# Kernel tuning notes

Measured on AMD Instinct MI355X. Metric: run time of the kernel, lower is better.

Reference implementation:

```python
import jax, jax.numpy as jnp
import numpy as np

D_IN = 1024
D_OUT = 1024
NUM_HEADS = 16
HEAD_DIM = D_OUT // NUM_HEADS


def setup_inputs() -> dict:
    key = jax.random.key(0)
    ks = jax.random.split(key, 6)
    B, T = 2, 2048
    x = jax.random.normal(ks[0], (B, T, D_IN), dtype=jnp.float32)
    s = 1.0 / np.sqrt(D_IN)
    Wq = jax.random.normal(ks[1], (D_IN, D_OUT), dtype=jnp.float32) * s
    Wk = jax.random.normal(ks[2], (D_IN, D_OUT), dtype=jnp.float32) * s
    Wv = jax.random.normal(ks[3], (D_IN, D_OUT), dtype=jnp.float32) * s
    Wo = jax.random.normal(ks[4], (D_OUT, D_OUT), dtype=jnp.float32) * (1.0 / np.sqrt(D_OUT))
    bo = jnp.zeros((D_OUT,), dtype=jnp.float32)
    return {"x": x, "Wq": Wq, "Wk": Wk, "Wv": Wv, "Wo": Wo, "bo": bo}


def reference(x, Wq, Wk, Wv, Wo, bo):
    B, T, _ = x.shape
    # project and split heads -> (B, H, T, Dh)
    def split(t):
        return t.reshape(B, T, NUM_HEADS, HEAD_DIM).transpose(0, 2, 1, 3)
    Q = split(x @ Wq)
    K = split(x @ Wk)
    V = split(x @ Wv)
    scale = HEAD_DIM ** -0.5
    scores = jnp.einsum('bhqd,bhkd->bhqk', Q, K) * scale  # (B,H,T,T)
    causal = jnp.triu(jnp.ones((T, T), dtype=bool), k=1)
    scores = jnp.where(causal, -jnp.inf, scores)
    weights = jax.nn.softmax(scores, axis=-1)
    ctx = jnp.einsum('bhqk,bhkd->bhqd', weights, V)  # (B,H,T,Dh)
    ctx = ctx.transpose(0, 2, 1, 3).reshape(B, T, D_OUT)
    return ctx @ Wo + bo
```

## Files before the change

### kernel.cpp

```cpp
#include <hip/hip_runtime.h>
#include <hip/hip_bf16.h>

#define NH   16
#define HD   64
#define BB   2
#define TT   2048
#define DIN  1024
#define DOUT 1024
#define MTOT (BB*TT)

#define QSCALE 0.18033688011112042f
#define MAXC   20.0f

typedef __hip_bfloat16 bf16;
typedef short bf16x8  __attribute__((ext_vector_type(8)));
typedef float f32x4   __attribute__((ext_vector_type(4)));
typedef float f32x16  __attribute__((ext_vector_type(16)));

__device__ __forceinline__ bf16 f2bf(float f){ return __float2bfloat16(f); }

__device__ __forceinline__ void gld16(const bf16* g, bf16* l){
    __builtin_amdgcn_global_load_lds(
        (const __attribute__((address_space(1))) unsigned int*)g,
        (__attribute__((address_space(3))) unsigned int*)l,
        16, 0, 0);
}

__device__ __forceinline__ size_t qk_off(int bh, int t, int d){
    return (size_t)bh*131072 + (size_t)(((t>>5)*4 + (d>>4))*512)
         + ((t&31) + 32*((d>>3)&1))*8 + (d&7);
}
__device__ __forceinline__ size_t v_off(int bh, int t, int d){
    return (size_t)bh*131072 + (size_t)((((t>>4)*2) + (d>>5))*512)
         + ((d&31) + 32*((t>>2)&1))*8 + ((t&3) + 4*((t>>3)&1));
}

__global__ void prep_all(const float* __restrict__ x,
                         const float* __restrict__ Wq, const float* __restrict__ Wk,
                         const float* __restrict__ Wv, const float* __restrict__ Wo,
                         bf16* __restrict__ xb, bf16* __restrict__ WT){
    __shared__ float tile[64][65];
    const int blk = blockIdx.x;
    if (blk < 4096){
        int i = blk*256 + threadIdx.x;
        float4 v = ((const float4*)x)[i];
        bf16 o[4] = {f2bf(v.x), f2bf(v.y), f2bf(v.z), f2bf(v.w)};
        *(ushort4*)&xb[(size_t)i*4] = *(ushort4*)o;
        return;
    }
    const int wb = blk - 4096;
    const int n0 = (wb >> 4) * 64, k0 = (wb & 15) * 64;
    const float* W;
    switch (n0 >> 10){ case 0: W=Wq; break; case 1: W=Wk; break; case 2: W=Wv; break; default: W=Wo; }
    const int c0 = n0 & 1023;
    const int tr = threadIdx.x >> 6;
    const int tc = threadIdx.x & 63;
    #pragma unroll
    for (int it = 0; it < 16; it++){
        int k = k0 + it*4 + tr;
        tile[it*4 + tr][tc] = W[(size_t)k*DOUT + c0 + tc];
    }
    __syncthreads();
    #pragma unroll
    for (int it = 0; it < 16; it++){
        int n = it*4 + tr;
        WT[(size_t)(n0 + n)*DIN + k0 + tc] = f2bf(tile[tc][n]);
    }
}

__launch_bounds__(512, 2)
__global__ void gemm_qkv(const bf16* __restrict__ Xb, const bf16* __restrict__ WT,
                         bf16* __restrict__ Qf, bf16* __restrict__ Kf, bf16* __restrict__ Vf){
    __shared__ __align__(16) bf16 As[2*256*64];
    __shared__ __align__(16) bf16 Bs[2*192*64];
    const int n0 = blockIdx.x * 192;
    const int m0 = blockIdx.y * 256;
    const int tid = threadIdx.x;
    const int wave = tid >> 6, lane = tid & 63;
    const int wr = wave >> 1;
    const int wc = wave & 1;
    const int quad = lane >> 4, l16 = lane & 15;
    const int srow = tid >> 3;
    const int schk = tid & 7;
    const int gcol = (schk ^ (srow & 7)) << 3;

    f32x4 acc[4][6] = {};

    auto stage = [&](int kt, int dbuf){
        const int k0 = kt * 64;
        bf16* Ad = &As[dbuf * 16384];
        bf16* Bd = &Bs[dbuf * 12288];
        #pragma unroll
        for (int j = 0; j < 4; j++){
            int r = srow + j*64;
            gld16(&Xb[(size_t)(m0 + r)*DIN + k0 + gcol], Ad + r*64 + schk*8);
        }
        #pragma unroll
        for (int j = 0; j < 3; j++){
            int r = srow + j*64;
            gld16(&WT[(size_t)(n0 + r)*DIN + k0 + gcol], Bd + r*64 + schk*8);
        }
    };

    auto compute = [&](int dbuf){
        const bf16* Ab = &As[dbuf * 16384];
        const bf16* Bb = &Bs[dbuf * 12288];
        bf16x8 af[4][2];
        #pragma unroll
        for (int mi = 0; mi < 4; mi++){
            int row = wr*64 + mi*16 + l16;
            af[mi][0] = *(const bf16x8*)&Ab[row*64 + (((quad    ) ^ (row & 7)) << 3)];
            af[mi][1] = *(const bf16x8*)&Ab[row*64 + (((4 + quad) ^ (row & 7)) << 3)];
        }
        #pragma unroll
        for (int ni = 0; ni < 6; ni++){
            int row = wc*96 + ni*16 + l16;
            bf16x8 b0 = *(const bf16x8*)&Bb[row*64 + (((quad    ) ^ (row & 7)) << 3)];
            bf16x8 b1 = *(const bf16x8*)&Bb[row*64 + (((4 + quad) ^ (row & 7)) << 3)];
            #pragma unroll
            for (int mi = 0; mi < 4; mi++){
                acc[mi][ni] = __builtin_amdgcn_mfma_f32_16x16x32_bf16(af[mi][0], b0, acc[mi][ni], 0, 0, 0);
                acc[mi][ni] = __builtin_amdgcn_mfma_f32_16x16x32_bf16(af[mi][1], b1, acc[mi][ni], 0, 0, 0);
            }
        }
    };

    stage(0, 0);

    for (int t = 0; t < 15; t++){
        const int buf = t & 1;
        stage(t + 1, buf ^ 1);
        asm volatile("s_waitcnt vmcnt(7)" ::: "memory");
        __builtin_amdgcn_s_barrier();
        compute(buf);
        asm volatile("s_waitcnt lgkmcnt(0)" ::: "memory");
        __builtin_amdgcn_s_barrier();
    }
    asm volatile("s_waitcnt vmcnt(0)" ::: "memory");
    __builtin_amdgcn_s_barrier();
    compute(1);

    #pragma unroll
    for (int mi = 0; mi < 4; mi++){
        #pragma unroll
        for (int ni = 0; ni < 6; ni++){
            int col = n0 + wc*96 + ni*16 + l16;
            int which = col >> 10;
            int c = col & 1023;
            int h = c >> 6, d = c & 63;
            int m_base = m0 + wr*64 + mi*16 + quad*4;
            int b = m_base >> 11, t0 = m_base & 2047;
            int bh = b*NH + h;
            if (which == 2){
                bf16 pk[4];
                #pragma unroll
                for (int r = 0; r < 4; r++) pk[r] = f2bf(acc[mi][ni][r]);
                *(ushort4*)&Vf[v_off(bh, t0, d)] = *(ushort4*)pk;
            } else if (which == 0){
                #pragma unroll
                for (int r = 0; r < 4; r++)
                    Qf[qk_off(bh, t0 + r, d)] = f2bf(acc[mi][ni][r] * QSCALE);
            } else {
                #pragma unroll
                for (int r = 0; r < 4; r++)
                    Kf[qk_off(bh, t0 + r, d)] = f2bf(acc[mi][ni][r]);
            }
        }
    }
}

__launch_bounds__(256, 4)
__global__ void attn(const bf16* __restrict__ Qf, const bf16* __restrict__ Kf,
                     const bf16* __restrict__ Vf, bf16* __restrict__ ctx){
    __shared__ float Lo[3*64*36];
    __shared__ float Ls[3*64];
    const int blk  = blockIdx.x;
    const int bh   = (blk & 7) + 8*((blk >> 3) & 3);
    const int qb   = 63 - (blk >> 5);
    const int wave = threadIdx.x >> 6, lane = threadIdx.x & 63;
    const int n    = qb + 1;
    const int tstart = (n*wave) >> 2;
    const int tend   = ((n*(wave+1)) >> 2) - 1;
    const int h32  = lane >> 5, l32 = lane & 31;
    const int b    = bh >> 4, head = bh & 15;
    const bf16* Qb = Qf + (size_t)bh*131072 + lane*8;
    const bf16* Kb = Kf + (size_t)bh*131072 + lane*8;
    const bf16* Vb = Vf + (size_t)bh*131072 + lane*8;

    bf16x8 qf[4];
    #pragma unroll
    for (int ks = 0; ks < 4; ks++)
        qf[ks] = *(const bf16x8*)(Qb + (qb*4 + ks)*512);

    bf16x8 kc[4], vc[4];
    #pragma unroll
    for (int i = 0; i < 4; i++){
        kc[i] = *(const bf16x8*)(Kb + (tstart*4 + i)*512);
        vc[i] = *(const bf16x8*)(Vb + (tstart*4 + i)*512);
    }

    f32x16 o0 = {}, o1 = {};
    float lsum = 0.f;

    for (int tb = tstart; tb <= tend; tb++){
        f32x16 s = {};
        #pragma unroll
        for (int ks = 0; ks < 4; ks++)
            s = __builtin_amdgcn_mfma_f32_32x32x16_bf16(kc[ks], qf[ks], s, 0, 0, 0);
        if (tb < tend){
            #pragma unroll
            for (int i = 0; i < 4; i++)
                kc[i] = *(const bf16x8*)(Kb + ((tb+1)*4 + i)*512);
        }
        if (tb == qb){
            #pragma unroll
            for (int r = 0; r < 16; r++){
                int trow = (r&3) + 8*(r>>2) + 4*h32;
                if (trow > l32) s[r] = -1e30f;
            }
        }
        float p[16];
        #pragma unroll
        for (int r = 0; r < 16; r++){
            p[r] = __builtin_amdgcn_exp2f(s[r] - MAXC);
            lsum += p[r];
        }
        #pragma unroll
        for (int ki = 0; ki < 2; ki++){
            bf16 pb[8];
            #pragma unroll
            for (int j = 0; j < 8; j++) pb[j] = f2bf(p[ki*8 + j]);
            bf16x8 pbv = *(bf16x8*)pb;
            o0 = __builtin_amdgcn_mfma_f32_32x32x16_bf16(vc[ki*2+0], pbv, o0, 0, 0, 0);
            o1 = __builtin_amdgcn_mfma_f32_32x32x16_bf16(vc[ki*2+1], pbv, o1, 0, 0, 0);
        }
        if (tb < tend){
            #pragma unroll
            for (int i = 0; i < 4; i++)
                vc[i] = *(const bf16x8*)(Vb + ((tb+1)*4 + i)*512);
        }
    }

    if (wave != 0){
        float* lo = &Lo[(wave-1)*2304 + lane*36];
        #pragma unroll
        for (int c = 0; c < 4; c++){
            f32x4 w4 = { o0[c*4+0], o0[c*4+1], o0[c*4+2], o0[c*4+3] };
            *(f32x4*)&lo[c*4] = w4;
        }
        #pragma unroll
        for (int c = 0; c < 4; c++){
            f32x4 w4 = { o1[c*4+0], o1[c*4+1], o1[c*4+2], o1[c*4+3] };
            *(f32x4*)&lo[16 + c*4] = w4;
        }
        Ls[(wave-1)*64 + lane] = lsum;
    }
    __syncthreads();
    if (wave == 0){
        float lc = lsum;
        #pragma unroll
        for (int w = 0; w < 3; w++){
            const float* lo = &Lo[w*2304 + lane*36];
            #pragma unroll
            for (int c = 0; c < 4; c++){
                f32x4 r4 = *(const f32x4*)&lo[c*4];
                #pragma unroll
                for (int i = 0; i < 4; i++) o0[c*4+i] += r4[i];
            }
            #pragma unroll
            for (int c = 0; c < 4; c++){
                f32x4 r4 = *(const f32x4*)&lo[16 + c*4];
                #pragma unroll
                for (int i = 0; i < 4; i++) o1[c*4+i] += r4[i];
            }
            lc += Ls[w*64 + lane];
        }
        float lq  = lc + __shfl_xor(lc, 32);
        float inv = 1.0f / lq;
        const int q = qb*32 + l32;
        bf16* cp = ctx + ((size_t)(b*TT + q))*DOUT + head*HD;
        #pragma unroll
        for (int db = 0; db < 2; db++){
            #pragma unroll
            for (int rq = 0; rq < 4; rq++){
                bf16 pk[4];
                #pragma unroll
                for (int i = 0; i < 4; i++){
                    float ov = (db ? o1[rq*4 + i] : o0[rq*4 + i]) * inv;
                    pk[i] = f2bf(ov);
                }
                int d0 = db*32 + rq*8 + h32*4;
                *(ushort4*)&cp[d0] = *(ushort4*)pk;
            }
        }
    }
}

__launch_bounds__(256)
__global__ void gemm_out(const bf16* __restrict__ Cx, const bf16* __restrict__ WoT,
                         const float* __restrict__ bo, float* __restrict__ out){
    __shared__ __align__(16) bf16 As[128*64];
    __shared__ __align__(16) bf16 Bs[64*64];
    const int n0 = blockIdx.x * 64;
    const int m0 = blockIdx.y * 128;
    const int tid = threadIdx.x;
    const int wave = tid >> 6, lane = tid & 63;
    const int wm = (wave & 1) * 64, wn = (wave >> 1) * 32;
    const int quad = lane >> 4, l16 = lane & 15;
    const int srow = wave*8 + (lane >> 3);
    const int schk = lane & 7;

    f32x4 acc[4][2] = {};
    for (int k0 = 0; k0 < DOUT; k0 += 64){
        #pragma unroll
        for (int j = 0; j < 4; j++){
            int r = srow + j*32;
            int gc = (schk ^ (r & 7)) << 3;
            gld16(&Cx[(size_t)(m0 + r)*DOUT + k0 + gc], &As[r*64 + schk*8]);
        }
        #pragma unroll
        for (int j = 0; j < 2; j++){
            int r = srow + j*32;
            int gc = (schk ^ (r & 7)) << 3;
            gld16(&WoT[(size_t)(n0 + r)*DOUT + k0 + gc], &Bs[r*64 + schk*8]);
        }
        __syncthreads();
        #pragma unroll
        for (int ks = 0; ks < 2; ks++){
            bf16x8 af[4], bfr[2];
            #pragma unroll
            for (int mi = 0; mi < 4; mi++){
                int row = wm + mi*16 + l16;
                af[mi] = *(bf16x8*)&As[row*64 + (((ks*4 + quad) ^ (row & 7)) << 3)];
            }
            #pragma unroll
            for (int ni = 0; ni < 2; ni++){
                int row = wn + ni*16 + l16;
                bfr[ni] = *(bf16x8*)&Bs[row*64 + (((ks*4 + quad) ^ (row & 7)) << 3)];
            }
            #pragma unroll
            for (int mi = 0; mi < 4; mi++)
                #pragma unroll
                for (int ni = 0; ni < 2; ni++)
                    acc[mi][ni] = __builtin_amdgcn_mfma_f32_16x16x32_bf16(af[mi], bfr[ni], acc[mi][ni], 0, 0, 0);
        }
        __syncthreads();
    }
    #pragma unroll
    for (int mi = 0; mi < 4; mi++){
        #pragma unroll
        for (int ni = 0; ni < 2; ni++){
            int nn = n0 + wn + ni*16 + l16;
            float bias = bo[nn];
            #pragma unroll
            for (int r = 0; r < 4; r++){
                int m = m0 + wm + mi*16 + quad*4 + r;
                out[(size_t)m*DOUT + nn] = acc[mi][ni][r] + bias;
            }
        }
    }
}

extern "C" void kernel_launch(void* const* d_in, const int* in_sizes, int n_in,
                              void* d_out, int out_size, void* d_ws, size_t ws_size,
                              hipStream_t stream){
    const float* x  = (const float*)d_in[0];
    const float* Wq = (const float*)d_in[1];
    const float* Wk = (const float*)d_in[2];
    const float* Wv = (const float*)d_in[3];
    const float* Wo = (const float*)d_in[4];
    const float* bo = (const float*)d_in[5];
    float* out = (float*)d_out;

    char* ws = (char*)d_ws;
    bf16* xb  = (bf16*)(ws);
    bf16* WT  = (bf16*)(ws + ((size_t)8  << 20));
    bf16* Qf  = (bf16*)(ws + ((size_t)16 << 20));
    bf16* Kf  = (bf16*)(ws + ((size_t)24 << 20));
    bf16* Vf  = (bf16*)(ws + ((size_t)32 << 20));
    bf16* ctx = (bf16*)(ws + ((size_t)40 << 20));
    bf16* WoT = WT + (size_t)3072*DIN;

    prep_all <<<dim3(5120),    256, 0, stream>>>(x, Wq, Wk, Wv, Wo, xb, WT);
    gemm_qkv <<<dim3(16, 16),  512, 0, stream>>>(xb, WT, Qf, Kf, Vf);
    attn     <<<dim3(2048),    256, 0, stream>>>(Qf, Kf, Vf, ctx);
    gemm_out <<<dim3(16, 32),  256, 0, stream>>>(ctx, WoT, bo, out);
}
```

Before: 164.5 us.

## Double-buffer output projection GEMM and widen tile to 128x128

The output projection GEMM now uses two LDS buffers so the next K tile's global-to-LDS loads are issued before computing on the current tile, with explicit vmcnt waits and barriers. The N tile grows from 64 to 128, so each wave accumulates a 4x4 block of MFMA outputs and the grid halves to 8x32 blocks. This aims to hide load latency and raise operand reuse per LDS read. The cost is more LDS and accumulator registers per block (launch bounds ask for 2 blocks/CU) and fewer blocks in flight.

```diff
diff --git a/kernel.cpp b/kernel.cpp
--- a/kernel.cpp
+++ b/kernel.cpp
@@ -296,60 +296,77 @@
     }
 }
 
-__launch_bounds__(256)
+__launch_bounds__(256, 2)
 __global__ void gemm_out(const bf16* __restrict__ Cx, const bf16* __restrict__ WoT,
                          const float* __restrict__ bo, float* __restrict__ out){
-    __shared__ __align__(16) bf16 As[128*64];
-    __shared__ __align__(16) bf16 Bs[64*64];
-    const int n0 = blockIdx.x * 64;
+    __shared__ __align__(16) bf16 As[2*128*64];
+    __shared__ __align__(16) bf16 Bs[2*128*64];
+    const int n0 = blockIdx.x * 128;
     const int m0 = blockIdx.y * 128;
     const int tid = threadIdx.x;
     const int wave = tid >> 6, lane = tid & 63;
-    const int wm = (wave & 1) * 64, wn = (wave >> 1) * 32;
+    const int wm = (wave & 1) * 64, wn = (wave >> 1) * 64;
     const int quad = lane >> 4, l16 = lane & 15;
-    const int srow = wave*8 + (lane >> 3);
-    const int schk = lane & 7;
-
-    f32x4 acc[4][2] = {};
-    for (int k0 = 0; k0 < DOUT; k0 += 64){
+    const int srow = tid >> 3;
+    const int schk = tid & 7;
+    const int gcol = (schk ^ (srow & 7)) << 3;
+
+    f32x4 acc[4][4] = {};
+
+    auto stage = [&](int kt, int dbuf){
+        const int k0 = kt * 64;
+        bf16* Ad = &As[dbuf * 8192];
+        bf16* Bd = &Bs[dbuf * 8192];
         #pragma unroll
         for (int j = 0; j < 4; j++){
             int r = srow + j*32;
-            int gc = (schk ^ (r & 7)) << 3;
-            gld16(&Cx[(size_t)(m0 + r)*DOUT + k0 + gc], &As[r*64 + schk*8]);
-        }
-        #pragma unroll
-        for (int j = 0; j < 2; j++){
-            int r = srow + j*32;
-            int gc = (schk ^ (r & 7)) << 3;
-            gld16(&WoT[(size_t)(n0 + r)*DOUT + k0 + gc], &Bs[r*64 + schk*8]);
-        }
-        __syncthreads();
+            gld16(&Cx[(size_t)(m0 + r)*DOUT + k0 + gcol], Ad + r*64 + schk*8);
+            gld16(&WoT[(size_t)(n0 + r)*DOUT + k0 + gcol], Bd + r*64 + schk*8);
+        }
+    };
+
+    auto compute = [&](int dbuf){
+        const bf16* Ab = &As[dbuf * 8192];
+        const bf16* Bb = &Bs[dbuf * 8192];
         #pragma unroll
         for (int ks = 0; ks < 2; ks++){
-            bf16x8 af[4], bfr[2];
+            bf16x8 af[4], bfr[4];
             #pragma unroll
             for (int mi = 0; mi < 4; mi++){
                 int row = wm + mi*16 + l16;
-                af[mi] = *(bf16x8*)&As[row*64 + (((ks*4 + quad) ^ (row & 7)) << 3)];
-            }
-            #pragma unroll
-            for (int ni = 0; ni < 2; ni++){
+                af[mi] = *(const bf16x8*)&Ab[row*64 + (((ks*4 + quad) ^ (row & 7)) << 3)];
+            }
+            #pragma unroll
+            for (int ni = 0; ni < 4; ni++){
                 int row = wn + ni*16 + l16;
-                bfr[ni] = *(bf16x8*)&Bs[row*64 + (((ks*4 + quad) ^ (row & 7)) << 3)];
+                bfr[ni] = *(const bf16x8*)&Bb[row*64 + (((ks*4 + quad) ^ (row & 7)) << 3)];
             }
             #pragma unroll
             for (int mi = 0; mi < 4; mi++)
                 #pragma unroll
-                for (int ni = 0; ni < 2; ni++)
+                for (int ni = 0; ni < 4; ni++)
                     acc[mi][ni] = __builtin_amdgcn_mfma_f32_16x16x32_bf16(af[mi], bfr[ni], acc[mi][ni], 0, 0, 0);
         }
-        __syncthreads();
-    }
+    };
+
+    stage(0, 0);
+    for (int t = 0; t < 15; t++){
+        const int buf = t & 1;
+        stage(t + 1, buf ^ 1);
+        asm volatile("s_waitcnt vmcnt(8)" ::: "memory");
+        __builtin_amdgcn_s_barrier();
+        compute(buf);
+        asm volatile("s_waitcnt lgkmcnt(0)" ::: "memory");
+        __builtin_amdgcn_s_barrier();
+    }
+    asm volatile("s_waitcnt vmcnt(0)" ::: "memory");
+    __builtin_amdgcn_s_barrier();
+    compute(1);
+
     #pragma unroll
     for (int mi = 0; mi < 4; mi++){
         #pragma unroll
-        for (int ni = 0; ni < 2; ni++){
+        for (int ni = 0; ni < 4; ni++){
             int nn = n0 + wn + ni*16 + l16;
             float bias = bo[nn];
             #pragma unroll
@@ -384,5 +401,5 @@
     prep_all <<<dim3(5120),    256, 0, stream>>>(x, Wq, Wk, Wv, Wo, xb, WT);
     gemm_qkv <<<dim3(16, 16),  512, 0, stream>>>(xb, WT, Qf, Kf, Vf);
     attn     <<<dim3(2048),    256, 0, stream>>>(Qf, Kf, Vf, ctx);
-    gemm_out <<<dim3(16, 32),  256, 0, stream>>>(ctx, WoT, bo, out);
-}
+    gemm_out <<<dim3(8, 32),   256, 0, stream>>>(ctx, WoT, bo, out);
+}
```

Result: slower. 170.3 us (+3.5%).
